# Kernel optimization log

Hardware: AMD Instinct MI355X
Metric: run time of the kernel (lower is better)

## Reference

```python
import jax, jax.numpy as jnp
import numpy as np

HIDDEN = 4096
NUM_HEADS = 32
HEAD_DIM = HIDDEN // NUM_HEADS  # 128, used only as softmax scale
CACHE_LEN = 100
BATCH = 8192


def setup_inputs() -> dict:
    key = jax.random.key(0)
    ks = jax.random.split(key, 7)
    return {
        "x": jax.random.normal(ks[0], (BATCH, HIDDEN), dtype=jnp.float32),
        "q_w": jax.random.normal(ks[1], (HIDDEN, HIDDEN), dtype=jnp.float32) * (1.0 / np.sqrt(HIDDEN)),
        "q_b": jax.random.normal(ks[2], (HIDDEN,), dtype=jnp.float32) * 0.01,
        "k_cache": jax.random.normal(ks[3], (CACHE_LEN, HIDDEN), dtype=jnp.float32),
        "v_cache": jax.random.normal(ks[4], (CACHE_LEN, HIDDEN), dtype=jnp.float32),
        "out_w": jax.random.normal(ks[5], (HIDDEN, HIDDEN), dtype=jnp.float32) * (1.0 / np.sqrt(HIDDEN)),
        "out_b": jax.random.normal(ks[6], (HIDDEN,), dtype=jnp.float32) * 0.01,
    }


def reference(x, q_w, q_b, k_cache, v_cache, out_w, out_b):
    # q_proj: torch Linear -> x @ W^T + b
    q = x @ q_w.T + q_b                                   # [N, H]
    # concat one zero row onto each cache (kv_len = CACHE_LEN + 1)
    k = jnp.concatenate([k_cache, jnp.zeros_like(k_cache[:1])], axis=0)  # [L+1, H]
    v = jnp.concatenate([v_cache, jnp.zeros_like(v_cache[:1])], axis=0)  # [L+1, H]
    scale = 1.0 / np.sqrt(HEAD_DIM).astype(np.float32)
    scores = (q @ k.T) * scale                            # [N, L+1]
    weights = jax.nn.softmax(scores, axis=-1)
    attn = weights @ v                                    # [N, H]
    return attn @ out_w.T + out_b                         # [N, H]
```

## Files before the change

### kernel.cpp

```cpp
#include <hip/hip_runtime.h>
#include <cstdio>

typedef __attribute__((ext_vector_type(8))) short short8;
typedef __attribute__((ext_vector_type(4))) float f32x4;


__device__ __forceinline__ unsigned short bf16r(float f) {
  union { float f; unsigned int u; } x; x.f = f;
  unsigned int r = x.u + 0x7fffu + ((x.u >> 16) & 1u);
  return (unsigned short)(r >> 16);
}

__device__ __forceinline__ float bf16f(unsigned short h) {
  union { unsigned int u; float f; } x; x.u = ((unsigned int)h) << 16;
  return x.f;
}

__device__ __forceinline__ void gload_lds16(const void* g, void* l) {
  __builtin_amdgcn_global_load_lds((const __attribute__((address_space(1))) void*)g,
                                   (__attribute__((address_space(3))) void*)l,
                                   16, 0, 0);
}

__device__ __forceinline__ short8 pack_bf16(float4 f0, float4 f1) {
  short8 h;
  h[0] = (short)bf16r(f0.x); h[1] = (short)bf16r(f0.y);
  h[2] = (short)bf16r(f0.z); h[3] = (short)bf16r(f0.w);
  h[4] = (short)bf16r(f1.x); h[5] = (short)bf16r(f1.y);
  h[6] = (short)bf16r(f1.z); h[7] = (short)bf16r(f1.w);
  return h;
}


__global__ void transpose_hilo(const float* __restrict__ in, unsigned short* __restrict__ out) {
  __shared__ float tile[64][65];
  const int j0 = blockIdx.x * 64, i0 = blockIdx.y * 64;
  const int tx = threadIdx.x & 15, ty = threadIdx.x >> 4;
  #pragma unroll
  for (int w = 0; w < 4; ++w) {
    int r = ty + w * 16;
    float4 v = *reinterpret_cast<const float4*>(in + (size_t)(i0 + r) * 4096 + j0 + tx * 4);
    tile[r][tx * 4 + 0] = v.x; tile[r][tx * 4 + 1] = v.y;
    tile[r][tx * 4 + 2] = v.z; tile[r][tx * 4 + 3] = v.w;
  }
  __syncthreads();
  #pragma unroll
  for (int w = 0; w < 4; ++w) {
    int r = ty + w * 16;
    float v0 = tile[tx * 4 + 0][r], v1 = tile[tx * 4 + 1][r];
    float v2 = tile[tx * 4 + 2][r], v3 = tile[tx * 4 + 3][r];
    ushort4 hi, lo;
    hi.x = bf16r(v0); lo.x = bf16r(v0 - bf16f(hi.x));
    hi.y = bf16r(v1); lo.y = bf16r(v1 - bf16f(hi.y));
    hi.z = bf16r(v2); lo.z = bf16r(v2 - bf16f(hi.z));
    hi.w = bf16r(v3); lo.w = bf16r(v3 - bf16f(hi.w));
    *reinterpret_cast<ushort4*>(out + (size_t)(j0 + r) * 8192 + i0 + tx * 4) = hi;
    *reinterpret_cast<ushort4*>(out + (size_t)(j0 + r) * 8192 + 4096 + i0 + tx * 4) = lo;
  }
}


__global__ void build_pad_dup(const float* __restrict__ src, unsigned short* __restrict__ dst) {
  int idx = blockIdx.x * blockDim.x + threadIdx.x;
  if (idx >= 128 * 4096) return;
  int l = idx >> 12, i = idx & 4095;
  float v = (l < 100) ? src[idx] : 0.f;
  unsigned short b = bf16r(v);
  dst[(size_t)l * 8192 + i] = b;
  dst[(size_t)l * 8192 + 4096 + i] = b;
}

__global__ void build_pad128(const float* __restrict__ src, unsigned short* __restrict__ dst) {
  int idx = blockIdx.x * blockDim.x + threadIdx.x;
  if (idx >= 128 * 4096) return;
  int row = idx >> 12;
  float v = (row < 100) ? src[idx] : 0.f;
  dst[idx] = bf16r(v);
}

__global__ void kq_bias(const float* __restrict__ kc, const float* __restrict__ qb,
                        float* __restrict__ sbias) {
  int l = blockIdx.x;
  int lane = threadIdx.x;
  float s = 0.f;
  if (l < 100) {
    for (int i = lane * 4; i < 4096; i += 256) {
      float4 k = *reinterpret_cast<const float4*>(kc + (size_t)l * 4096 + i);
      float4 q = *reinterpret_cast<const float4*>(qb + i);
      s += k.x * q.x + k.y * q.y + k.z * q.z + k.w * q.w;
    }
  }
  #pragma unroll
  for (int off = 1; off < 64; off <<= 1) s += __shfl_xor(s, off);
  if (lane == 0) sbias[l] = s;
}


__global__ void gemm_ntk_splitk(const unsigned short* __restrict__ A,
                                const unsigned short* __restrict__ B,
                                float* __restrict__ Cpart,
                                int M, int N, int Kstride, int kchunk) {
  __shared__ unsigned short As[128][32];
  __shared__ unsigned short Bs[128][32];

  const int tid = threadIdx.x, wave = tid >> 6, lane = tid & 63;
  const int wm = wave >> 1, wn = wave & 1;
  const size_t rowA0 = (size_t)blockIdx.y * 128;
  const size_t colB0 = (size_t)blockIdx.z * 128;
  const int k0base = blockIdx.x * kchunk;

  f32x4 acc[4][4] = {};

  const int sr = wave * 16 + (lane >> 2);
  const int sc = (lane & 3) << 3;

  const unsigned short* Ap0 = A + (rowA0 + sr) * (size_t)Kstride + k0base + sc;
  const unsigned short* Ap1 = A + (rowA0 + 64 + sr) * (size_t)Kstride + k0base + sc;
  const unsigned short* Bp0 = B + (colB0 + sr) * (size_t)Kstride + k0base + sc;
  const unsigned short* Bp1 = B + (colB0 + 64 + sr) * (size_t)Kstride + k0base + sc;
  unsigned short* AsD0 = &As[wave * 16][0];
  unsigned short* AsD1 = &As[64 + wave * 16][0];
  unsigned short* BsD0 = &Bs[wave * 16][0];
  unsigned short* BsD1 = &Bs[64 + wave * 16][0];

  const int fr = lane & 15;
  const int fk = (lane >> 4) << 3;

  for (int k0 = 0; k0 < kchunk; k0 += 32) {
    gload_lds16(Ap0 + k0, AsD0);
    gload_lds16(Ap1 + k0, AsD1);
    gload_lds16(Bp0 + k0, BsD0);
    gload_lds16(Bp1 + k0, BsD1);
    __syncthreads();

    short8 av[4], bv[4];
    #pragma unroll
    for (int mi = 0; mi < 4; ++mi)
      av[mi] = *reinterpret_cast<const short8*>(&As[wm * 64 + mi * 16 + fr][fk]);
    #pragma unroll
    for (int ni = 0; ni < 4; ++ni)
      bv[ni] = *reinterpret_cast<const short8*>(&Bs[wn * 64 + ni * 16 + fr][fk]);
    #pragma unroll
    for (int mi = 0; mi < 4; ++mi)
      #pragma unroll
      for (int ni = 0; ni < 4; ++ni)
        acc[mi][ni] = __builtin_amdgcn_mfma_f32_16x16x32_bf16(av[mi], bv[ni], acc[mi][ni], 0, 0, 0);
    __syncthreads();
  }

  float* Cp = Cpart + (size_t)blockIdx.x * M * N;
  const int orow = (lane >> 4) * 4;
  const int ocol = lane & 15;
  #pragma unroll
  for (int mi = 0; mi < 4; ++mi) {
    #pragma unroll
    for (int ni = 0; ni < 4; ++ni) {
      size_t r0 = rowA0 + wm * 64 + mi * 16 + orow;
      size_t c  = colB0 + wn * 64 + ni * 16 + ocol;
      #pragma unroll
      for (int j = 0; j < 4; ++j)
        Cp[(r0 + j) * (size_t)N + c] = acc[mi][ni][j];
    }
  }
}


template<int NB>
__global__ __launch_bounds__(256, 1)
void gemm_sv(const float* __restrict__ A, const unsigned short* __restrict__ B,
             float* __restrict__ Cpart, int M, int Kstride, int kchunk) {
  constexpr int FOLD = NB / 128;
  __shared__ float          As[2][128][32];
  __shared__ unsigned short Bs[2][NB][32];

  const int tid = threadIdx.x, wave = tid >> 6, lane = tid & 63;
  const int wm = wave >> 1, wn = wave & 1;
  const int ks = blockIdx.x, mblk = blockIdx.y;
  const size_t rowA0 = (size_t)mblk * 128;
  const int k0 = ks * kchunk;
  const int nsteps = kchunk >> 5;

  const int ar = lane >> 3;
  const int as_g = (lane & 7) ^ ar;
  const int br = lane >> 2;
  const int bs_g = (lane & 3) ^ (br & 3);

#define STAGE_SV(kt, BUF) do { \
    const int _kc = k0 + (kt) * 32; \
    _Pragma("unroll") \
    for (int j = 0; j < 4; ++j) \
      gload_lds16(A + (rowA0 + wave * 32 + j * 8 + ar) * (size_t)Kstride + _kc + as_g * 4, \
                  &As[BUF][wave * 32 + j * 8][0]); \
    _Pragma("unroll") \
    for (int j = 0; j < NB / 64; ++j) \
      gload_lds16(B + (size_t)(wave * (NB / 4) + j * 16 + br) * Kstride + _kc + bs_g * 8, \
                  &Bs[BUF][wave * (NB / 4) + j * 16][0]); \
  } while (0)

#define WAIT_STAGE do { \
    if (NB == 256) asm volatile("s_waitcnt vmcnt(8)" ::: "memory"); \
    else           asm volatile("s_waitcnt vmcnt(6)" ::: "memory"); \
  } while (0)

  const int fr = lane & 15, kq = lane >> 4;
  f32x4 acc[4][4] = {};

  STAGE_SV(0, 0);
  STAGE_SV(1, 1);
  WAIT_STAGE;
  asm volatile("" ::: "memory");
  __builtin_amdgcn_s_barrier();
  asm volatile("" ::: "memory");

  for (int k = 0; k < nsteps; ++k) {
    const int c = k & 1;

    short8 av[4], bv[4][FOLD];
    #pragma unroll
    for (int mi = 0; mi < 4; ++mi) {
      const float* rp = &As[c][wm * 64 + mi * 16 + fr][0];
      float4 f0 = *reinterpret_cast<const float4*>(rp + (((2 * kq)     ^ (fr & 7)) * 4));
      float4 f1 = *reinterpret_cast<const float4*>(rp + (((2 * kq + 1) ^ (fr & 7)) * 4));
      av[mi] = pack_bf16(f0, f1);
    }
    #pragma unroll
    for (int ni = 0; ni < 4; ++ni)
      #pragma unroll
      for (int p = 0; p < FOLD; ++p) {
        int rb = p * 128 + wn * 64 + ni * 16 + fr;
        bv[ni][p] = *reinterpret_cast<const short8*>(&Bs[c][rb][0] + ((kq ^ (fr & 3)) * 8));
      }

    asm volatile("s_waitcnt lgkmcnt(0)" ::: "memory");
    __builtin_amdgcn_s_barrier();
    asm volatile("" ::: "memory");

    const int kt2 = (k + 2 < nsteps) ? k + 2 : nsteps - 1;
    STAGE_SV(kt2, c);
    asm volatile("" ::: "memory");

    __builtin_amdgcn_s_setprio(1);
    #pragma unroll
    for (int mi = 0; mi < 4; ++mi)
      #pragma unroll
      for (int ni = 0; ni < 4; ++ni)
        #pragma unroll
        for (int p = 0; p < FOLD; ++p)
          acc[mi][ni] = __builtin_amdgcn_mfma_f32_16x16x32_bf16(av[mi], bv[ni][p], acc[mi][ni], 0, 0, 0);
    __builtin_amdgcn_s_setprio(0);

    WAIT_STAGE;
    asm volatile("" ::: "memory");
    __builtin_amdgcn_s_barrier();
    asm volatile("" ::: "memory");
  }

#undef STAGE_SV
#undef WAIT_STAGE

  float* Cp = Cpart + (size_t)ks * M * 128;
  const int orow = (lane >> 4) * 4;
  const int ocol = lane & 15;
  #pragma unroll
  for (int mi = 0; mi < 4; ++mi) {
    #pragma unroll
    for (int ni = 0; ni < 4; ++ni) {
      size_t r0 = rowA0 + wm * 64 + mi * 16 + orow;
      size_t c  = (size_t)wn * 64 + ni * 16 + ocol;
      #pragma unroll
      for (int j = 0; j < 4; ++j)
        Cp[(r0 + j) * 128 + c] = acc[mi][ni][j];
    }
  }
}


__global__ void kq_reduce(const float* __restrict__ KQpart, unsigned short* __restrict__ KQ2) {
  int idx = blockIdx.x * blockDim.x + threadIdx.x;
  if (idx >= 128 * 4096) return;
  float s = 0.f;
  #pragma unroll
  for (int ks = 0; ks < 8; ++ks) s += KQpart[(size_t)ks * 128 * 4096 + idx];
  unsigned short hi = bf16r(s);
  unsigned short lo = bf16r(s - bf16f(hi));
  int l = idx >> 12, j = idx & 4095;
  KQ2[(size_t)l * 4096 + j]         = hi;
  KQ2[(size_t)(l + 128) * 4096 + j] = lo;
}


__global__ void softmax_fused2(const float* __restrict__ Spart, const float* __restrict__ sbias,
                               unsigned short* __restrict__ W2, int rows) {
  int wave = threadIdx.x >> 6;
  int lane = threadIdx.x & 63;
  int row = blockIdx.x * (blockDim.x >> 6) + wave;
  if (row >= rows) return;
  const float scale = 0.088388347648318447f;
  float sx = 0.f, sy = 0.f;
  #pragma unroll
  for (int ks = 0; ks < 8; ++ks) {
    float2 p = reinterpret_cast<const float2*>(Spart + ((size_t)ks * rows + row) * 128)[lane];
    sx += p.x; sy += p.y;
  }
  float2 bb = reinterpret_cast<const float2*>(sbias)[lane];
  sx += bb.x; sy += bb.y;
  int c0 = lane * 2, c1 = c0 + 1;
  float s0 = (c0 <= 100) ? sx * scale : -1e30f;
  float s1 = (c1 <= 100) ? sy * scale : -1e30f;
  float m = fmaxf(s0, s1);
  #pragma unroll
  for (int off = 1; off < 64; off <<= 1) m = fmaxf(m, __shfl_xor(m, off));
  float e0 = (c0 <= 100) ? __expf(s0 - m) : 0.f;
  float e1 = (c1 <= 100) ? __expf(s1 - m) : 0.f;
  float sum = e0 + e1;
  #pragma unroll
  for (int off = 1; off < 64; off <<= 1) sum += __shfl_xor(sum, off);
  float inv = 1.f / sum;
  ushort2 o;
  o.x = bf16r(e0 * inv);
  o.y = bf16r(e1 * inv);
  reinterpret_cast<ushort2*>(W2 + (size_t)row * 256)[lane] = o;
  reinterpret_cast<ushort2*>(W2 + (size_t)row * 256 + 128)[lane] = o;
}


__global__ void vo_reduce(const float* __restrict__ VOpart, unsigned short* __restrict__ VOT2) {
  int idx = blockIdx.x * blockDim.x + threadIdx.x;
  if (idx >= 4096 * 128) return;
  float s = 0.f;
  #pragma unroll
  for (int ks = 0; ks < 16; ++ks) s += VOpart[(size_t)ks * 4096 * 128 + idx];
  unsigned short hi = bf16r(s);
  unsigned short lo = bf16r(s - bf16f(hi));
  int o = idx >> 7, l = idx & 127;
  VOT2[(size_t)o * 256 + l]       = hi;
  VOT2[(size_t)o * 256 + 128 + l] = lo;
}


__global__ __launch_bounds__(256)
void gemm_final(const unsigned short* __restrict__ A,
                const unsigned short* __restrict__ B,
                const float* __restrict__ bias,
                float* __restrict__ Cout,
                int M, int N, int K) {
  __shared__ unsigned short As[128][40];
  __shared__ unsigned short Bs[128][40];

  const int tid = threadIdx.x, wave = tid >> 6, lane = tid & 63;
  const int wm = wave >> 1, wn = wave & 1;
  const size_t rowA0 = (size_t)blockIdx.y * 128;
  const size_t colB0 = (size_t)blockIdx.x * 128;

  f32x4 acc[4][4] = {};

  const int srow  = tid >> 1;
  const int shalf = (tid & 1) * 16;

  const unsigned short* Ap = A + (rowA0 + srow) * (size_t)K + shalf;
  const unsigned short* Bp = B + (colB0 + srow) * (size_t)K + shalf;

  const int fr = lane & 15;
  const int fk = (lane >> 4) << 3;

  for (int k0 = 0; k0 < K; k0 += 32) {
    short8 a0 = *reinterpret_cast<const short8*>(Ap + k0);
    short8 a1 = *reinterpret_cast<const short8*>(Ap + k0 + 8);
    short8 b0 = *reinterpret_cast<const short8*>(Bp + k0);
    short8 b1 = *reinterpret_cast<const short8*>(Bp + k0 + 8);
    *reinterpret_cast<short8*>(&As[srow][shalf])     = a0;
    *reinterpret_cast<short8*>(&As[srow][shalf + 8]) = a1;
    *reinterpret_cast<short8*>(&Bs[srow][shalf])     = b0;
    *reinterpret_cast<short8*>(&Bs[srow][shalf + 8]) = b1;
    __syncthreads();

    short8 av[4], bv[4];
    #pragma unroll
    for (int mi = 0; mi < 4; ++mi)
      av[mi] = *reinterpret_cast<const short8*>(&As[wm * 64 + mi * 16 + fr][fk]);
    #pragma unroll
    for (int ni = 0; ni < 4; ++ni)
      bv[ni] = *reinterpret_cast<const short8*>(&Bs[wn * 64 + ni * 16 + fr][fk]);
    #pragma unroll
    for (int mi = 0; mi < 4; ++mi)
      #pragma unroll
      for (int ni = 0; ni < 4; ++ni)
        acc[mi][ni] = __builtin_amdgcn_mfma_f32_16x16x32_bf16(av[mi], bv[ni], acc[mi][ni], 0, 0, 0);
    __syncthreads();
  }

  const int orow = (lane >> 4) * 4;
  const int ocol = lane & 15;
  #pragma unroll
  for (int mi = 0; mi < 4; ++mi) {
    #pragma unroll
    for (int ni = 0; ni < 4; ++ni) {
      size_t r0 = rowA0 + wm * 64 + mi * 16 + orow;
      size_t c  = colB0 + wn * 64 + ni * 16 + ocol;
      float bv_ = bias[c];
      #pragma unroll
      for (int j = 0; j < 4; ++j)
        Cout[(r0 + j) * (size_t)N + c] = acc[mi][ni][j] + bv_;
    }
  }
}


extern "C" void kernel_launch(void* const* d_in, const int* in_sizes, int n_in,
                              void* d_out, int out_size, void* d_ws, size_t ws_size,
                              hipStream_t stream) {
  const float* x       = (const float*)d_in[0];
  const float* q_w     = (const float*)d_in[1];
  const float* q_b     = (const float*)d_in[2];
  const float* k_cache = (const float*)d_in[3];
  const float* v_cache = (const float*)d_in[4];
  const float* out_w   = (const float*)d_in[5];
  const float* out_b   = (const float*)d_in[6];
  float* out = (float*)d_out;

  const int M = 8192, H = 4096;

  char* ws = (char*)d_ws;
  size_t off = 0;
  auto alloc = [&](size_t bytes) { void* p = ws + off; off += (bytes + 255) & ~(size_t)255; return p; };
  unsigned short* qwt2   = (unsigned short*)alloc((size_t)H * 8192 * 2);
  unsigned short* kpad2  = (unsigned short*)alloc((size_t)128 * 8192 * 2);
  unsigned short* vpad   = (unsigned short*)alloc((size_t)128 * H * 2);
  float*          sbias  = (float*)alloc(128 * 4);
  unsigned short* KQ2    = (unsigned short*)alloc((size_t)256 * H * 2);
  unsigned short* W2     = (unsigned short*)alloc((size_t)M * 256 * 2);
  unsigned short* VOT2   = (unsigned short*)alloc((size_t)H * 256 * 2);
  float*          scratch= (float*)alloc((size_t)36 << 20);
  if (ws_size < off) { fprintf(stderr, "ws too small: need %zu have %zu\n", off, ws_size); return; }

  transpose_hilo<<<dim3(64, 64), 256, 0, stream>>>(q_w, qwt2);
  build_pad_dup<<<2048, 256, 0, stream>>>(k_cache, kpad2);
  build_pad128<<<2048, 256, 0, stream>>>(v_cache, vpad);
  kq_bias<<<128, 64, 0, stream>>>(k_cache, q_b, sbias);

  gemm_ntk_splitk<<<dim3(8, 1, 32), 256, 0, stream>>>(kpad2, qwt2, scratch, 128, H, 8192, 1024);
  kq_reduce<<<2048, 256, 0, stream>>>(scratch, KQ2);

  gemm_sv<256><<<dim3(8, 64), 256, 0, stream>>>(x, KQ2, scratch, M, H, 512);

  softmax_fused2<<<M / 4, 256, 0, stream>>>(scratch, sbias, W2, M);

  gemm_sv<128><<<dim3(16, 32), 256, 0, stream>>>(out_w, vpad, scratch, H, H, 256);
  vo_reduce<<<2048, 256, 0, stream>>>(scratch, VOT2);

  gemm_final<<<dim3(32, 64), 256, 0, stream>>>(W2, VOT2, out_b, out, M, H, 256);
}
```

Measured before the change: 201.5 us.

## Fuse q_w transpose and hi/lo bf16 split into the K·Qw GEMM

Measured after the change: 188.4 us. -6.5%, faster.

```diff
diff --git a/kernel.cpp b/kernel.cpp
--- a/kernel.cpp
+++ b/kernel.cpp
@@ -31,44 +31,6 @@
   return h;
 }
 
-
-__global__ void transpose_hilo(const float* __restrict__ in, unsigned short* __restrict__ out) {
-  __shared__ float tile[64][65];
-  const int j0 = blockIdx.x * 64, i0 = blockIdx.y * 64;
-  const int tx = threadIdx.x & 15, ty = threadIdx.x >> 4;
-  #pragma unroll
-  for (int w = 0; w < 4; ++w) {
-    int r = ty + w * 16;
-    float4 v = *reinterpret_cast<const float4*>(in + (size_t)(i0 + r) * 4096 + j0 + tx * 4);
-    tile[r][tx * 4 + 0] = v.x; tile[r][tx * 4 + 1] = v.y;
-    tile[r][tx * 4 + 2] = v.z; tile[r][tx * 4 + 3] = v.w;
-  }
-  __syncthreads();
-  #pragma unroll
-  for (int w = 0; w < 4; ++w) {
-    int r = ty + w * 16;
-    float v0 = tile[tx * 4 + 0][r], v1 = tile[tx * 4 + 1][r];
-    float v2 = tile[tx * 4 + 2][r], v3 = tile[tx * 4 + 3][r];
-    ushort4 hi, lo;
-    hi.x = bf16r(v0); lo.x = bf16r(v0 - bf16f(hi.x));
-    hi.y = bf16r(v1); lo.y = bf16r(v1 - bf16f(hi.y));
-    hi.z = bf16r(v2); lo.z = bf16r(v2 - bf16f(hi.z));
-    hi.w = bf16r(v3); lo.w = bf16r(v3 - bf16f(hi.w));
-    *reinterpret_cast<ushort4*>(out + (size_t)(j0 + r) * 8192 + i0 + tx * 4) = hi;
-    *reinterpret_cast<ushort4*>(out + (size_t)(j0 + r) * 8192 + 4096 + i0 + tx * 4) = lo;
-  }
-}
-
-
-__global__ void build_pad_dup(const float* __restrict__ src, unsigned short* __restrict__ dst) {
-  int idx = blockIdx.x * blockDim.x + threadIdx.x;
-  if (idx >= 128 * 4096) return;
-  int l = idx >> 12, i = idx & 4095;
-  float v = (l < 100) ? src[idx] : 0.f;
-  unsigned short b = bf16r(v);
-  dst[(size_t)l * 8192 + i] = b;
-  dst[(size_t)l * 8192 + 4096 + i] = b;
-}
 
 __global__ void build_pad128(const float* __restrict__ src, unsigned short* __restrict__ dst) {
   int idx = blockIdx.x * blockDim.x + threadIdx.x;
@@ -96,70 +58,91 @@
 }
 
 
-__global__ void gemm_ntk_splitk(const unsigned short* __restrict__ A,
-                                const unsigned short* __restrict__ B,
-                                float* __restrict__ Cpart,
-                                int M, int N, int Kstride, int kchunk) {
-  __shared__ unsigned short As[128][32];
-  __shared__ unsigned short Bs[128][32];
+__global__ __launch_bounds__(256)
+void kq_fused(const unsigned short* __restrict__ Kp,
+              const float* __restrict__ Qw,
+              float* __restrict__ Cpart,
+              int H, int jchunk) {
+  __shared__ unsigned short Ak[128][32];
+  __shared__ float Ts[32][129];
 
   const int tid = threadIdx.x, wave = tid >> 6, lane = tid & 63;
   const int wm = wave >> 1, wn = wave & 1;
-  const size_t rowA0 = (size_t)blockIdx.y * 128;
-  const size_t colB0 = (size_t)blockIdx.z * 128;
-  const int k0base = blockIdx.x * kchunk;
-
-  f32x4 acc[4][4] = {};
+  const int j0 = blockIdx.x * jchunk;
+  const int i0 = blockIdx.y * 128;
 
   const int sr = wave * 16 + (lane >> 2);
   const int sc = (lane & 3) << 3;
-
-  const unsigned short* Ap0 = A + (rowA0 + sr) * (size_t)Kstride + k0base + sc;
-  const unsigned short* Ap1 = A + (rowA0 + 64 + sr) * (size_t)Kstride + k0base + sc;
-  const unsigned short* Bp0 = B + (colB0 + sr) * (size_t)Kstride + k0base + sc;
-  const unsigned short* Bp1 = B + (colB0 + 64 + sr) * (size_t)Kstride + k0base + sc;
-  unsigned short* AsD0 = &As[wave * 16][0];
-  unsigned short* AsD1 = &As[64 + wave * 16][0];
-  unsigned short* BsD0 = &Bs[wave * 16][0];
-  unsigned short* BsD1 = &Bs[64 + wave * 16][0];
+  const unsigned short* Kp0 = Kp + (size_t)sr * H + j0 + sc;
+  const unsigned short* Kp1 = Kp + (size_t)(64 + sr) * H + j0 + sc;
+  unsigned short* AD0 = &Ak[wave * 16][0];
+  unsigned short* AD1 = &Ak[64 + wave * 16][0];
+
+  const int tj = tid >> 3;
+  const int tc = (tid & 7) * 16;
+  const float* Qp = Qw + (size_t)(j0 + tj) * H + i0 + tc;
 
   const int fr = lane & 15;
-  const int fk = (lane >> 4) << 3;
-
-  for (int k0 = 0; k0 < kchunk; k0 += 32) {
-    gload_lds16(Ap0 + k0, AsD0);
-    gload_lds16(Ap1 + k0, AsD1);
-    gload_lds16(Bp0 + k0, BsD0);
-    gload_lds16(Bp1 + k0, BsD1);
+  const int kq = lane >> 4;
+
+  f32x4 acc[4][4] = {};
+
+  for (int jj = 0; jj < jchunk; jj += 32) {
+    gload_lds16(Kp0 + jj, AD0);
+    gload_lds16(Kp1 + jj, AD1);
+    {
+      const float* q = Qp + (size_t)jj * H;
+      float4 v0 = *reinterpret_cast<const float4*>(q);
+      float4 v1 = *reinterpret_cast<const float4*>(q + 4);
+      float4 v2 = *reinterpret_cast<const float4*>(q + 8);
+      float4 v3 = *reinterpret_cast<const float4*>(q + 12);
+      Ts[tj][tc + 0]  = v0.x; Ts[tj][tc + 1]  = v0.y; Ts[tj][tc + 2]  = v0.z; Ts[tj][tc + 3]  = v0.w;
+      Ts[tj][tc + 4]  = v1.x; Ts[tj][tc + 5]  = v1.y; Ts[tj][tc + 6]  = v1.z; Ts[tj][tc + 7]  = v1.w;
+      Ts[tj][tc + 8]  = v2.x; Ts[tj][tc + 9]  = v2.y; Ts[tj][tc + 10] = v2.z; Ts[tj][tc + 11] = v2.w;
+      Ts[tj][tc + 12] = v3.x; Ts[tj][tc + 13] = v3.y; Ts[tj][tc + 14] = v3.z; Ts[tj][tc + 15] = v3.w;
+    }
     __syncthreads();
 
-    short8 av[4], bv[4];
+    short8 av[4];
     #pragma unroll
     for (int mi = 0; mi < 4; ++mi)
-      av[mi] = *reinterpret_cast<const short8*>(&As[wm * 64 + mi * 16 + fr][fk]);
-    #pragma unroll
-    for (int ni = 0; ni < 4; ++ni)
-      bv[ni] = *reinterpret_cast<const short8*>(&Bs[wn * 64 + ni * 16 + fr][fk]);
+      av[mi] = *reinterpret_cast<const short8*>(&Ak[wm * 64 + mi * 16 + fr][kq * 8]);
+
+    short8 bhi[4], blo[4];
+    #pragma unroll
+    for (int ni = 0; ni < 4; ++ni) {
+      const int ic = wn * 64 + ni * 16 + fr;
+      #pragma unroll
+      for (int s = 0; s < 8; ++s) {
+        float f = Ts[kq * 8 + s][ic];
+        unsigned short h = bf16r(f);
+        bhi[ni][s] = (short)h;
+        blo[ni][s] = (short)bf16r(f - bf16f(h));
+      }
+    }
+
     #pragma unroll
     for (int mi = 0; mi < 4; ++mi)
       #pragma unroll
-      for (int ni = 0; ni < 4; ++ni)
-        acc[mi][ni] = __builtin_amdgcn_mfma_f32_16x16x32_bf16(av[mi], bv[ni], acc[mi][ni], 0, 0, 0);
+      for (int ni = 0; ni < 4; ++ni) {
+        acc[mi][ni] = __builtin_amdgcn_mfma_f32_16x16x32_bf16(av[mi], bhi[ni], acc[mi][ni], 0, 0, 0);
+        acc[mi][ni] = __builtin_amdgcn_mfma_f32_16x16x32_bf16(av[mi], blo[ni], acc[mi][ni], 0, 0, 0);
+      }
     __syncthreads();
   }
 
-  float* Cp = Cpart + (size_t)blockIdx.x * M * N;
+  float* Cp = Cpart + (size_t)blockIdx.x * 128 * H;
   const int orow = (lane >> 4) * 4;
   const int ocol = lane & 15;
   #pragma unroll
   for (int mi = 0; mi < 4; ++mi) {
     #pragma unroll
     for (int ni = 0; ni < 4; ++ni) {
-      size_t r0 = rowA0 + wm * 64 + mi * 16 + orow;
-      size_t c  = colB0 + wn * 64 + ni * 16 + ocol;
+      size_t r0 = (size_t)wm * 64 + mi * 16 + orow;
+      size_t c  = (size_t)i0 + wn * 64 + ni * 16 + ocol;
       #pragma unroll
       for (int j = 0; j < 4; ++j)
-        Cp[(r0 + j) * (size_t)N + c] = acc[mi][ni][j];
+        Cp[(r0 + j) * (size_t)H + c] = acc[mi][ni][j];
     }
   }
 }
@@ -423,8 +406,7 @@
   char* ws = (char*)d_ws;
   size_t off = 0;
   auto alloc = [&](size_t bytes) { void* p = ws + off; off += (bytes + 255) & ~(size_t)255; return p; };
-  unsigned short* qwt2   = (unsigned short*)alloc((size_t)H * 8192 * 2);
-  unsigned short* kpad2  = (unsigned short*)alloc((size_t)128 * 8192 * 2);
+  unsigned short* kpad   = (unsigned short*)alloc((size_t)128 * H * 2);
   unsigned short* vpad   = (unsigned short*)alloc((size_t)128 * H * 2);
   float*          sbias  = (float*)alloc(128 * 4);
   unsigned short* KQ2    = (unsigned short*)alloc((size_t)256 * H * 2);
@@ -433,12 +415,11 @@
   float*          scratch= (float*)alloc((size_t)36 << 20);
   if (ws_size < off) { fprintf(stderr, "ws too small: need %zu have %zu\n", off, ws_size); return; }
 
-  transpose_hilo<<<dim3(64, 64), 256, 0, stream>>>(q_w, qwt2);
-  build_pad_dup<<<2048, 256, 0, stream>>>(k_cache, kpad2);
+  build_pad128<<<2048, 256, 0, stream>>>(k_cache, kpad);
   build_pad128<<<2048, 256, 0, stream>>>(v_cache, vpad);
   kq_bias<<<128, 64, 0, stream>>>(k_cache, q_b, sbias);
 
-  gemm_ntk_splitk<<<dim3(8, 1, 32), 256, 0, stream>>>(kpad2, qwt2, scratch, 128, H, 8192, 1024);
+  kq_fused<<<dim3(8, 32), 256, 0, stream>>>(kpad, q_w, scratch, H, 512);
   kq_reduce<<<2048, 256, 0, stream>>>(scratch, KQ2);
 
   gemm_sv<256><<<dim3(8, 64), 256, 0, stream>>>(x, KQ2, scratch, M, H, 512);
```
